# Performance work log

Hardware: AMD Instinct MI355X
Metric: run time of the kernel (lower is better)

## Reference

```python
import jax, jax.numpy as jnp
import numpy as np

N_NODES = 50000
N_EDGES = 640000
D = 128


def setup_inputs() -> dict:
    key = jax.random.key(0)
    k1, k2, k3, k4, k5 = jax.random.split(key, 5)
    graph_embedding = jax.random.normal(k1, (N_NODES, D), dtype=jnp.float32)
    # xavier_uniform for a (1, D) tensor: bound = sqrt(6/(1+D))
    bound = float(np.sqrt(6.0 / (1 + D)))
    weight = jax.random.uniform(k2, (1, D), dtype=jnp.float32, minval=-bound, maxval=bound)
    e_feat = jax.random.randint(k3, (N_EDGES,), 0, 31, dtype=jnp.int64)
    src = jax.random.randint(k4, (N_EDGES,), 0, N_NODES, dtype=jnp.int64)
    dst = jax.random.randint(k5, (N_EDGES,), 0, N_NODES, dtype=jnp.int64)
    return {"graph_embedding": graph_embedding, "weight": weight,
            "e_feat": e_feat, "src": src, "dst": dst}


def reference(graph_embedding, weight, e_feat, src, dst):
    n_nodes = graph_embedding.shape[0]
    # emb == ft == ft0 == ft1 == ft2 == ft3 in the original module
    emb = jax.nn.elu(graph_embedding * weight)  # [N, D]
    e = e_feat.reshape(-1, 1).astype(jnp.float32)  # [E, 1] (module casts to float)
    # res + sum_k where(e==type_k, ft_k, 0) with all ft_k identical ->
    # per-edge multiplier 1 + matched-type indicators
    mult = (1.0
            + (e == 0.0).astype(emb.dtype)
            + (e == 6.0).astype(emb.dtype)
            + (e == 14.0).astype(emb.dtype)
            + (e == 30.0).astype(emb.dtype))  # [E, 1]
    msgs = emb[src] * mult  # [E, D] gather + mask-select
    # fn.sum('m','ft'): scatter-add messages to destination nodes
    return jax.ops.segment_sum(msgs, dst, num_segments=n_nodes)  # [N, D]
```

## Files before the change

kernel.cpp:

```cpp
#include <hip/hip_runtime.h>

#define D      128
#define NT     256
#define KB     320
#define CAPBB  64
#define NBMAX  256

typedef __attribute__((ext_vector_type(4))) _Float16 half4;
typedef __attribute__((ext_vector_type(4))) float    f32x4;

__device__ __forceinline__ float4 elu_mul(float4 g, float4 w) {
    float4 v;
    v.x = g.x * w.x; v.y = g.y * w.y; v.z = g.z * w.z; v.w = g.w * w.w;
    v.x = (v.x > 0.0f) ? v.x : (__expf(v.x) - 1.0f);
    v.y = (v.y > 0.0f) ? v.y : (__expf(v.y) - 1.0f);
    v.z = (v.z > 0.0f) ? v.z : (__expf(v.z) - 1.0f);
    v.w = (v.w > 0.0f) ? v.w : (__expf(v.w) - 1.0f);
    return v;
}

__global__ __launch_bounds__(NT)
void fused_kernel(const float* __restrict__ ge, const float* __restrict__ weight,
                  const int* __restrict__ e_feat, const int* __restrict__ src,
                  const int* __restrict__ dst,
                  _Float16* __restrict__ emb, uint2* __restrict__ binned,
                  int* __restrict__ cnts, uint2* __restrict__ spill,
                  int* __restrict__ spill_cnt,
                  int n_nodes, int n_edges, int nbins, int per_block) {
    if ((int)blockIdx.x < KB) {
        __shared__ int rk[NBMAX];
        __shared__ int sp;
        int t = threadIdx.x;
        for (int i = t; i < NBMAX; i += NT) rk[i] = 0;
        if (t == 0) sp = 0;
        __syncthreads();

        int blk = blockIdx.x;
        int e0 = blk * per_block;
        int e1 = e0 + per_block; if (e1 > n_edges) e1 = n_edges;
        for (int e = e0 + t; e < e1; e += NT) {
            int d = dst[e];
            int b = d >> 8;
            int f = e_feat[e];
            unsigned int flag = (f == 0 || f == 6 || f == 14 || f == 30) ? 1u : 0u;
            unsigned int rec  = (unsigned int)src[e] | (flag << 31);
            int r = atomicAdd(&rk[b], 1);
            if (r < CAPBB) {
                binned[((size_t)blk * nbins + b) * CAPBB + r] =
                    make_uint2(rec, (unsigned int)(d & 255));
            } else {
                int s = atomicAdd(&sp, 1);
                spill[(size_t)blk * per_block + s] = make_uint2(rec, (unsigned int)d);
            }
        }
        __syncthreads();
        for (int b = t; b < nbins; b += NT)
            cnts[blk * nbins + b] = rk[b] < CAPBB ? rk[b] : CAPBB;
        if (t == 0) spill_cnt[blk] = sp;
    } else {
        int t = ((int)blockIdx.x - KB) * NT + threadIdx.x;
        int quads = n_nodes * (D / 4);
        if (t < quads) {
            int col = (t & 31) * 4;
            float4 g = *reinterpret_cast<const float4*>(ge + (size_t)t * 4);
            float4 w = *reinterpret_cast<const float4*>(weight + col);
            float4 v = elu_mul(g, w);
            half4 h;
            h.x = (_Float16)v.x; h.y = (_Float16)v.y;
            h.z = (_Float16)v.z; h.w = (_Float16)v.w;
            *reinterpret_cast<half4*>(emb + (size_t)t * 4) = h;
        }
    }
}

__global__ __launch_bounds__(1024)
void csr_kernel(const uint2* __restrict__ binned, const int* __restrict__ cnts,
                uint2* __restrict__ offdeg, unsigned int* __restrict__ bucket,
                const int* __restrict__ spill_cnt, int* __restrict__ spill_total,
                int n_nodes, int nbins, int capb_out) {
    __shared__ int cnt2[NBMAX];
    __shared__ int off2[NBMAX];
    __shared__ int rk2[NBMAX];
    __shared__ int cellc[KB];
    __shared__ int stot;
    int t = threadIdx.x;
    int b = blockIdx.x;

    for (int i = t; i < NBMAX; i += 1024) { cnt2[i] = 0; rk2[i] = 0; }
    if (t < KB) cellc[t] = cnts[t * nbins + b];
    if (t == 0) stot = 0;
    __syncthreads();

    if (t < KB) {
        const uint2* cell = binned + ((size_t)t * nbins + b) * CAPBB;
        int c = cellc[t];
        for (int j = 0; j < c; ++j) atomicAdd(&cnt2[cell[j].y], 1);
    }
    __syncthreads();

    if (t < NBMAX) off2[t] = cnt2[t];
    __syncthreads();
    for (int d2 = 1; d2 < NBMAX; d2 <<= 1) {
        int x = 0;
        if (t < NBMAX && t >= d2) x = off2[t - d2];
        __syncthreads();
        if (t < NBMAX) off2[t] += x;
        __syncthreads();
    }

    int G = b * capb_out;
    if (t < NBMAX) {
        int node = (b << 8) + t;
        if (node < n_nodes)
            offdeg[node] = make_uint2((unsigned int)(G + off2[t] - cnt2[t]),
                                      (unsigned int)cnt2[t]);
    }
    __syncthreads();

    if (t < KB) {
        const uint2* cell = binned + ((size_t)t * nbins + b) * CAPBB;
        int c = cellc[t];
        for (int j = 0; j < c; ++j) {
            uint2 r = cell[j];
            int l = (int)r.y;
            int p = atomicAdd(&rk2[l], 1);
            bucket[G + (off2[l] - cnt2[l]) + p] = r.x;
        }
    }

    if (b == 0) {
        if (t < KB && spill_cnt[t] > 0) atomicAdd(&stot, spill_cnt[t]);
        __syncthreads();
        if (t == 0) *spill_total = stot;
    }
}

__global__ __launch_bounds__(NT)
void gather_kernel(const _Float16* __restrict__ emb,
                   const uint2* __restrict__ offdeg,
                   const unsigned int* __restrict__ bucket,
                   const int* __restrict__ spill_total,
                   const int* __restrict__ spill_cnt,
                   const uint2* __restrict__ spill,
                   float* __restrict__ out, int n_nodes, int per_block) {
    int tid = blockIdx.x * NT + threadIdx.x;
    int node = tid >> 5;
    if (node >= n_nodes) return;
    int col = (tid & 31) * 4;

    uint2 od = offdeg[node];
    int beg = (int)od.x;
    int end = beg + (int)od.y;
    float4 acc = make_float4(0.f, 0.f, 0.f, 0.f);

    int i = beg;
    for (; i + 8 <= end; i += 8) {
        unsigned int r0 = bucket[i+0], r1 = bucket[i+1], r2 = bucket[i+2], r3 = bucket[i+3];
        unsigned int r4 = bucket[i+4], r5 = bucket[i+5], r6 = bucket[i+6], r7 = bucket[i+7];
        half4 h0 = *reinterpret_cast<const half4*>(emb + (size_t)(r0 & 0x7FFFFFFFu) * D + col);
        half4 h1 = *reinterpret_cast<const half4*>(emb + (size_t)(r1 & 0x7FFFFFFFu) * D + col);
        half4 h2 = *reinterpret_cast<const half4*>(emb + (size_t)(r2 & 0x7FFFFFFFu) * D + col);
        half4 h3 = *reinterpret_cast<const half4*>(emb + (size_t)(r3 & 0x7FFFFFFFu) * D + col);
        half4 h4 = *reinterpret_cast<const half4*>(emb + (size_t)(r4 & 0x7FFFFFFFu) * D + col);
        half4 h5 = *reinterpret_cast<const half4*>(emb + (size_t)(r5 & 0x7FFFFFFFu) * D + col);
        half4 h6 = *reinterpret_cast<const half4*>(emb + (size_t)(r6 & 0x7FFFFFFFu) * D + col);
        half4 h7 = *reinterpret_cast<const half4*>(emb + (size_t)(r7 & 0x7FFFFFFFu) * D + col);
        float m0 = (r0 >> 31) ? 2.f : 1.f, m1 = (r1 >> 31) ? 2.f : 1.f;
        float m2 = (r2 >> 31) ? 2.f : 1.f, m3 = (r3 >> 31) ? 2.f : 1.f;
        float m4 = (r4 >> 31) ? 2.f : 1.f, m5 = (r5 >> 31) ? 2.f : 1.f;
        float m6 = (r6 >> 31) ? 2.f : 1.f, m7 = (r7 >> 31) ? 2.f : 1.f;
        acc.x += (float)h0.x*m0 + (float)h1.x*m1 + (float)h2.x*m2 + (float)h3.x*m3
               + (float)h4.x*m4 + (float)h5.x*m5 + (float)h6.x*m6 + (float)h7.x*m7;
        acc.y += (float)h0.y*m0 + (float)h1.y*m1 + (float)h2.y*m2 + (float)h3.y*m3
               + (float)h4.y*m4 + (float)h5.y*m5 + (float)h6.y*m6 + (float)h7.y*m7;
        acc.z += (float)h0.z*m0 + (float)h1.z*m1 + (float)h2.z*m2 + (float)h3.z*m3
               + (float)h4.z*m4 + (float)h5.z*m5 + (float)h6.z*m6 + (float)h7.z*m7;
        acc.w += (float)h0.w*m0 + (float)h1.w*m1 + (float)h2.w*m2 + (float)h3.w*m3
               + (float)h4.w*m4 + (float)h5.w*m5 + (float)h6.w*m6 + (float)h7.w*m7;
    }
    for (; i + 4 <= end; i += 4) {
        unsigned int r0 = bucket[i+0], r1 = bucket[i+1], r2 = bucket[i+2], r3 = bucket[i+3];
        half4 h0 = *reinterpret_cast<const half4*>(emb + (size_t)(r0 & 0x7FFFFFFFu) * D + col);
        half4 h1 = *reinterpret_cast<const half4*>(emb + (size_t)(r1 & 0x7FFFFFFFu) * D + col);
        half4 h2 = *reinterpret_cast<const half4*>(emb + (size_t)(r2 & 0x7FFFFFFFu) * D + col);
        half4 h3 = *reinterpret_cast<const half4*>(emb + (size_t)(r3 & 0x7FFFFFFFu) * D + col);
        float m0 = (r0 >> 31) ? 2.f : 1.f, m1 = (r1 >> 31) ? 2.f : 1.f;
        float m2 = (r2 >> 31) ? 2.f : 1.f, m3 = (r3 >> 31) ? 2.f : 1.f;
        acc.x += (float)h0.x*m0 + (float)h1.x*m1 + (float)h2.x*m2 + (float)h3.x*m3;
        acc.y += (float)h0.y*m0 + (float)h1.y*m1 + (float)h2.y*m2 + (float)h3.y*m3;
        acc.z += (float)h0.z*m0 + (float)h1.z*m1 + (float)h2.z*m2 + (float)h3.z*m3;
        acc.w += (float)h0.w*m0 + (float)h1.w*m1 + (float)h2.w*m2 + (float)h3.w*m3;
    }
    for (; i < end; ++i) {
        unsigned int r = bucket[i];
        half4 h = *reinterpret_cast<const half4*>(emb + (size_t)(r & 0x7FFFFFFFu) * D + col);
        float m = (r >> 31) ? 2.f : 1.f;
        acc.x += (float)h.x*m; acc.y += (float)h.y*m;
        acc.z += (float)h.z*m; acc.w += (float)h.w*m;
    }

    if (*spill_total > 0) {
        for (int blk = 0; blk < KB; ++blk) {
            int sc = spill_cnt[blk];
            for (int j = 0; j < sc; ++j) {
                uint2 o = spill[(size_t)blk * per_block + j];
                if ((int)o.y == node) {
                    half4 h = *reinterpret_cast<const half4*>(emb + (size_t)(o.x & 0x7FFFFFFFu) * D + col);
                    float m = (o.x >> 31) ? 2.f : 1.f;
                    acc.x += (float)h.x*m; acc.y += (float)h.y*m;
                    acc.z += (float)h.z*m; acc.w += (float)h.w*m;
                }
            }
        }
    }

    f32x4 o;
    o.x = acc.x; o.y = acc.y; o.z = acc.z; o.w = acc.w;
    __builtin_nontemporal_store(o, reinterpret_cast<f32x4*>(out + (size_t)node * D + col));
}

__global__ void edge_scatter_fallback(const float* __restrict__ ge,
                                      const float* __restrict__ weight,
                                      const int* __restrict__ e_feat,
                                      const int* __restrict__ src,
                                      const int* __restrict__ dst,
                                      float* __restrict__ out, int n_edges) {
    long long tid = (long long)blockIdx.x * blockDim.x + threadIdx.x;
    int edge = (int)(tid >> 5);
    if (edge >= n_edges) return;
    int col = (int)(tid & 31) * 4;
    int e = e_feat[edge];
    float mult = (e == 0 || e == 6 || e == 14 || e == 30) ? 2.0f : 1.0f;
    float4 w = *reinterpret_cast<const float4*>(weight + col);
    float4 g = *reinterpret_cast<const float4*>(ge + (long long)src[edge] * D + col);
    float4 v = elu_mul(g, w);
    float* o = out + (long long)dst[edge] * D + col;
    atomicAdd(o + 0, v.x * mult);
    atomicAdd(o + 1, v.y * mult);
    atomicAdd(o + 2, v.z * mult);
    atomicAdd(o + 3, v.w * mult);
}

extern "C" void kernel_launch(void* const* d_in, const int* in_sizes, int n_in,
                              void* d_out, int out_size, void* d_ws, size_t ws_size,
                              hipStream_t stream) {
    const float* ge     = (const float*)d_in[0];
    const float* weight = (const float*)d_in[1];
    const int*   e_feat = (const int*)d_in[2];
    const int*   src    = (const int*)d_in[3];
    const int*   dst    = (const int*)d_in[4];
    float* out = (float*)d_out;

    int n_edges = in_sizes[2];
    int n_nodes = out_size / D;
    int nbins   = (n_nodes + 255) >> 8;
    int per_block = (n_edges + KB - 1) / KB;
    int capb_out  = KB * CAPBB;

    auto align256 = [](size_t x) { return (x + 255) & ~(size_t)255; };
    size_t o_emb    = 0;
    size_t o_binned = o_emb    + align256((size_t)n_nodes * D * sizeof(_Float16));
    size_t o_spill  = o_binned + align256((size_t)KB * nbins * CAPBB * 8);
    size_t o_cnts   = o_spill  + align256((size_t)KB * per_block * 8);
    size_t o_scnt   = o_cnts   + align256((size_t)KB * nbins * 4);
    size_t o_stot   = o_scnt   + align256((size_t)KB * 4);
    size_t o_offdeg = o_stot   + 256;
    size_t o_bucket = o_offdeg + align256((size_t)n_nodes * 8);
    size_t need     = o_bucket + align256((size_t)nbins * capb_out * 4);

    if (ws_size < need || nbins > NBMAX) {
        (void)hipMemsetAsync(d_out, 0, (size_t)out_size * sizeof(float), stream);
        long long total = (long long)n_edges * 32;
        edge_scatter_fallback<<<(int)((total + 255) / 256), 256, 0, stream>>>(
            ge, weight, e_feat, src, dst, out, n_edges);
        return;
    }

    char* ws = (char*)d_ws;
    _Float16*     emb     = (_Float16*)(ws + o_emb);
    uint2*        binned  = (uint2*)(ws + o_binned);
    uint2*        spill   = (uint2*)(ws + o_spill);
    int*          cnts    = (int*)(ws + o_cnts);
    int*          scnt    = (int*)(ws + o_scnt);
    int*          stot    = (int*)(ws + o_stot);
    uint2*        offdeg  = (uint2*)(ws + o_offdeg);
    unsigned int* bucket  = (unsigned int*)(ws + o_bucket);

    int quads = n_nodes * (D / 4);
    int embBlocks = (quads + NT - 1) / NT;

    fused_kernel<<<KB + embBlocks, NT, 0, stream>>>(
        ge, weight, e_feat, src, dst, emb, binned, cnts, spill, scnt,
        n_nodes, n_edges, nbins, per_block);
    csr_kernel<<<nbins, 1024, 0, stream>>>(binned, cnts, offdeg, bucket,
                                           scnt, stot, n_nodes, nbins, capb_out);

    long long total = (long long)n_nodes * 32;
    gather_kernel<<<(int)((total + 255) / 256), NT, 0, stream>>>(
        emb, offdeg, bucket, stot, scnt, spill, out, n_nodes, per_block);
}
```

Baseline: 57.13 us.

## Spread CSR cell scans over all threads and widen gather to 8 halves per lane

The CSR build kernel used to have one thread walk each bin cell serially, leaving most of the 1024 threads idle. It now assigns one thread per slot across all KB*CAPBB slots, with a bounds check against the cell count. The gather kernel now uses 16 lanes per node, each loading 8 fp16 values (16 bytes) instead of 4, halving thread count and doubling per-thread work. This trades fewer index loads and wider memory transactions for more registers and less thread-level parallelism in the gather. Per-node accumulation order changes slightly, and the bucket order within a node can now vary between runs because of the parallel slot scan.

```diff
diff --git a/kernel.cpp b/kernel.cpp
--- a/kernel.cpp
+++ b/kernel.cpp
@@ -7,6 +7,7 @@
 #define NBMAX  256
 
 typedef __attribute__((ext_vector_type(4))) _Float16 half4;
+typedef __attribute__((ext_vector_type(8))) _Float16 half8;
 typedef __attribute__((ext_vector_type(4))) float    f32x4;
 
 __device__ __forceinline__ float4 elu_mul(float4 g, float4 w) {
@@ -91,10 +92,15 @@
     if (t == 0) stot = 0;
     __syncthreads();
 
-    if (t < KB) {
-        const uint2* cell = binned + ((size_t)t * nbins + b) * CAPBB;
-        int c = cellc[t];
-        for (int j = 0; j < c; ++j) atomicAdd(&cnt2[cell[j].y], 1);
+    const int nslots = KB * CAPBB;
+
+    for (int slot = t; slot < nslots; slot += 1024) {
+        int cell = slot >> 6;
+        int j    = slot & (CAPBB - 1);
+        if (j < cellc[cell]) {
+            uint2 r = binned[((size_t)cell * nbins + b) * CAPBB + j];
+            atomicAdd(&cnt2[r.y], 1);
+        }
     }
     __syncthreads();
 
@@ -117,11 +123,11 @@
     }
     __syncthreads();
 
-    if (t < KB) {
-        const uint2* cell = binned + ((size_t)t * nbins + b) * CAPBB;
-        int c = cellc[t];
-        for (int j = 0; j < c; ++j) {
-            uint2 r = cell[j];
+    for (int slot = t; slot < nslots; slot += 1024) {
+        int cell = slot >> 6;
+        int j    = slot & (CAPBB - 1);
+        if (j < cellc[cell]) {
+            uint2 r = binned[((size_t)cell * nbins + b) * CAPBB + j];
             int l = (int)r.y;
             int p = atomicAdd(&rk2[l], 1);
             bucket[G + (off2[l] - cnt2[l]) + p] = r.x;
@@ -144,59 +150,57 @@
                    const uint2* __restrict__ spill,
                    float* __restrict__ out, int n_nodes, int per_block) {
     int tid = blockIdx.x * NT + threadIdx.x;
-    int node = tid >> 5;
+    int node = tid >> 4;
     if (node >= n_nodes) return;
-    int col = (tid & 31) * 4;
+    int col = (tid & 15) * 8;
 
     uint2 od = offdeg[node];
     int beg = (int)od.x;
     int end = beg + (int)od.y;
-    float4 acc = make_float4(0.f, 0.f, 0.f, 0.f);
+    float a0=0.f,a1=0.f,a2=0.f,a3=0.f,a4=0.f,a5=0.f,a6=0.f,a7=0.f;
+
+    const _Float16* ebase = emb + col;
+
+#define ACC8(h, m)                                                             \
+    a0 += (float)(h)[0]*(m); a1 += (float)(h)[1]*(m);                          \
+    a2 += (float)(h)[2]*(m); a3 += (float)(h)[3]*(m);                          \
+    a4 += (float)(h)[4]*(m); a5 += (float)(h)[5]*(m);                          \
+    a6 += (float)(h)[6]*(m); a7 += (float)(h)[7]*(m);
 
     int i = beg;
     for (; i + 8 <= end; i += 8) {
         unsigned int r0 = bucket[i+0], r1 = bucket[i+1], r2 = bucket[i+2], r3 = bucket[i+3];
         unsigned int r4 = bucket[i+4], r5 = bucket[i+5], r6 = bucket[i+6], r7 = bucket[i+7];
-        half4 h0 = *reinterpret_cast<const half4*>(emb + (size_t)(r0 & 0x7FFFFFFFu) * D + col);
-        half4 h1 = *reinterpret_cast<const half4*>(emb + (size_t)(r1 & 0x7FFFFFFFu) * D + col);
-        half4 h2 = *reinterpret_cast<const half4*>(emb + (size_t)(r2 & 0x7FFFFFFFu) * D + col);
-        half4 h3 = *reinterpret_cast<const half4*>(emb + (size_t)(r3 & 0x7FFFFFFFu) * D + col);
-        half4 h4 = *reinterpret_cast<const half4*>(emb + (size_t)(r4 & 0x7FFFFFFFu) * D + col);
-        half4 h5 = *reinterpret_cast<const half4*>(emb + (size_t)(r5 & 0x7FFFFFFFu) * D + col);
-        half4 h6 = *reinterpret_cast<const half4*>(emb + (size_t)(r6 & 0x7FFFFFFFu) * D + col);
-        half4 h7 = *reinterpret_cast<const half4*>(emb + (size_t)(r7 & 0x7FFFFFFFu) * D + col);
+        half8 h0 = *reinterpret_cast<const half8*>(ebase + (size_t)(r0 & 0x7FFFFFFFu) * D);
+        half8 h1 = *reinterpret_cast<const half8*>(ebase + (size_t)(r1 & 0x7FFFFFFFu) * D);
+        half8 h2 = *reinterpret_cast<const half8*>(ebase + (size_t)(r2 & 0x7FFFFFFFu) * D);
+        half8 h3 = *reinterpret_cast<const half8*>(ebase + (size_t)(r3 & 0x7FFFFFFFu) * D);
+        half8 h4 = *reinterpret_cast<const half8*>(ebase + (size_t)(r4 & 0x7FFFFFFFu) * D);
+        half8 h5 = *reinterpret_cast<const half8*>(ebase + (size_t)(r5 & 0x7FFFFFFFu) * D);
+        half8 h6 = *reinterpret_cast<const half8*>(ebase + (size_t)(r6 & 0x7FFFFFFFu) * D);
+        half8 h7 = *reinterpret_cast<const half8*>(ebase + (size_t)(r7 & 0x7FFFFFFFu) * D);
         float m0 = (r0 >> 31) ? 2.f : 1.f, m1 = (r1 >> 31) ? 2.f : 1.f;
         float m2 = (r2 >> 31) ? 2.f : 1.f, m3 = (r3 >> 31) ? 2.f : 1.f;
         float m4 = (r4 >> 31) ? 2.f : 1.f, m5 = (r5 >> 31) ? 2.f : 1.f;
         float m6 = (r6 >> 31) ? 2.f : 1.f, m7 = (r7 >> 31) ? 2.f : 1.f;
-        acc.x += (float)h0.x*m0 + (float)h1.x*m1 + (float)h2.x*m2 + (float)h3.x*m3
-               + (float)h4.x*m4 + (float)h5.x*m5 + (float)h6.x*m6 + (float)h7.x*m7;
-        acc.y += (float)h0.y*m0 + (float)h1.y*m1 + (float)h2.y*m2 + (float)h3.y*m3
-               + (float)h4.y*m4 + (float)h5.y*m5 + (float)h6.y*m6 + (float)h7.y*m7;
-        acc.z += (float)h0.z*m0 + (float)h1.z*m1 + (float)h2.z*m2 + (float)h3.z*m3
-               + (float)h4.z*m4 + (float)h5.z*m5 + (float)h6.z*m6 + (float)h7.z*m7;
-        acc.w += (float)h0.w*m0 + (float)h1.w*m1 + (float)h2.w*m2 + (float)h3.w*m3
-               + (float)h4.w*m4 + (float)h5.w*m5 + (float)h6.w*m6 + (float)h7.w*m7;
+        ACC8(h0, m0) ACC8(h1, m1) ACC8(h2, m2) ACC8(h3, m3)
+        ACC8(h4, m4) ACC8(h5, m5) ACC8(h6, m6) ACC8(h7, m7)
     }
     for (; i + 4 <= end; i += 4) {
         unsigned int r0 = bucket[i+0], r1 = bucket[i+1], r2 = bucket[i+2], r3 = bucket[i+3];
-        half4 h0 = *reinterpret_cast<const half4*>(emb + (size_t)(r0 & 0x7FFFFFFFu) * D + col);
-        half4 h1 = *reinterpret_cast<const half4*>(emb + (size_t)(r1 & 0x7FFFFFFFu) * D + col);
-        half4 h2 = *reinterpret_cast<const half4*>(emb + (size_t)(r2 & 0x7FFFFFFFu) * D + col);
-        half4 h3 = *reinterpret_cast<const half4*>(emb + (size_t)(r3 & 0x7FFFFFFFu) * D + col);
+        half8 h0 = *reinterpret_cast<const half8*>(ebase + (size_t)(r0 & 0x7FFFFFFFu) * D);
+        half8 h1 = *reinterpret_cast<const half8*>(ebase + (size_t)(r1 & 0x7FFFFFFFu) * D);
+        half8 h2 = *reinterpret_cast<const half8*>(ebase + (size_t)(r2 & 0x7FFFFFFFu) * D);
+        half8 h3 = *reinterpret_cast<const half8*>(ebase + (size_t)(r3 & 0x7FFFFFFFu) * D);
         float m0 = (r0 >> 31) ? 2.f : 1.f, m1 = (r1 >> 31) ? 2.f : 1.f;
         float m2 = (r2 >> 31) ? 2.f : 1.f, m3 = (r3 >> 31) ? 2.f : 1.f;
-        acc.x += (float)h0.x*m0 + (float)h1.x*m1 + (float)h2.x*m2 + (float)h3.x*m3;
-        acc.y += (float)h0.y*m0 + (float)h1.y*m1 + (float)h2.y*m2 + (float)h3.y*m3;
-        acc.z += (float)h0.z*m0 + (float)h1.z*m1 + (float)h2.z*m2 + (float)h3.z*m3;
-        acc.w += (float)h0.w*m0 + (float)h1.w*m1 + (float)h2.w*m2 + (float)h3.w*m3;
+        ACC8(h0, m0) ACC8(h1, m1) ACC8(h2, m2) ACC8(h3, m3)
     }
     for (; i < end; ++i) {
         unsigned int r = bucket[i];
-        half4 h = *reinterpret_cast<const half4*>(emb + (size_t)(r & 0x7FFFFFFFu) * D + col);
+        half8 h = *reinterpret_cast<const half8*>(ebase + (size_t)(r & 0x7FFFFFFFu) * D);
         float m = (r >> 31) ? 2.f : 1.f;
-        acc.x += (float)h.x*m; acc.y += (float)h.y*m;
-        acc.z += (float)h.z*m; acc.w += (float)h.w*m;
+        ACC8(h, m)
     }
 
     if (*spill_total > 0) {
@@ -205,18 +209,21 @@
             for (int j = 0; j < sc; ++j) {
                 uint2 o = spill[(size_t)blk * per_block + j];
                 if ((int)o.y == node) {
-                    half4 h = *reinterpret_cast<const half4*>(emb + (size_t)(o.x & 0x7FFFFFFFu) * D + col);
+                    half8 h = *reinterpret_cast<const half8*>(ebase + (size_t)(o.x & 0x7FFFFFFFu) * D);
                     float m = (o.x >> 31) ? 2.f : 1.f;
-                    acc.x += (float)h.x*m; acc.y += (float)h.y*m;
-                    acc.z += (float)h.z*m; acc.w += (float)h.w*m;
+                    ACC8(h, m)
                 }
             }
         }
     }
-
-    f32x4 o;
-    o.x = acc.x; o.y = acc.y; o.z = acc.z; o.w = acc.w;
-    __builtin_nontemporal_store(o, reinterpret_cast<f32x4*>(out + (size_t)node * D + col));
+#undef ACC8
+
+    float* obase = out + (size_t)node * D + col;
+    f32x4 lo, hi;
+    lo.x = a0; lo.y = a1; lo.z = a2; lo.w = a3;
+    hi.x = a4; hi.y = a5; hi.z = a6; hi.w = a7;
+    __builtin_nontemporal_store(lo, reinterpret_cast<f32x4*>(obase));
+    __builtin_nontemporal_store(hi, reinterpret_cast<f32x4*>(obase + 4));
 }
 
 __global__ void edge_scatter_fallback(const float* __restrict__ ge,
@@ -295,7 +302,7 @@
     csr_kernel<<<nbins, 1024, 0, stream>>>(binned, cnts, offdeg, bucket,
                                            scnt, stot, n_nodes, nbins, capb_out);
 
-    long long total = (long long)n_nodes * 32;
-    gather_kernel<<<(int)((total + 255) / 256), NT, 0, stream>>>(
+    long long total = (long long)n_nodes * 16;
+    gather_kernel<<<(int)((total + NT - 1) / NT), NT, 0, stream>>>(
         emb, offdeg, bucket, stot, scnt, spill, out, n_nodes, per_block);
 }
```

Result: slower. 61.29 us (+7.3%).
